# Performance work log

Hardware: AMD Instinct MI355X
Metric: run time of the kernel (lower is better)

## Reference

```python
import jax, jax.numpy as jnp
import numpy as np

# config (mirrors init_kwargs)
R = 1.0           # ball-query radius
K = 32            # ball-query neighbors
SPATIAL_STRIDE = 4
TKS = 3           # temporal kernel size (odd)
TPAD = (1, 1)     # replicate temporal padding
HEADS = 8
DIM_HEAD = 64
DIM = 512
MLP = 2048
DEPTH = 2
LN_EPS = 1e-5


def fps(xyz, m):
    # CUDA-style furthest point sampling, starts at index 0. xyz: [N,3] -> [m] int32
    N = xyz.shape[0]
    def body(carry, _):
        dists, last = carry
        d = jnp.sum((xyz - xyz[last]) ** 2, axis=-1)
        dists = jnp.minimum(dists, d)
        nxt = jnp.argmax(dists).astype(jnp.int32)
        return (dists, nxt), nxt
    init = (jnp.full((N,), 1e10, xyz.dtype), jnp.int32(0))
    _, idxs = jax.lax.scan(body, init, None, length=m - 1)
    return jnp.concatenate([jnp.zeros((1,), jnp.int32), idxs])


def ball_query(neighbor_xyz, anchor_xyz):
    # first K neighbor indices within radius R (pad with first found, 0 if none)
    N = neighbor_xyz.shape[0]
    d2 = jnp.sum((anchor_xyz[:, None, :] - neighbor_xyz[None, :, :]) ** 2, -1)  # [M,N]
    cand = jnp.where(d2 < R * R, jnp.arange(N, dtype=jnp.int32)[None, :], N)
    firstk = jnp.sort(cand, axis=-1)[:, :K]
    first = firstk[:, :1]
    idx = jnp.where(firstk >= N, first, firstk)
    return jnp.where(idx >= N, 0, idx).astype(jnp.int32)


def layer_norm(x, g, b):
    mu = jnp.mean(x, -1, keepdims=True)
    var = jnp.var(x, -1, keepdims=True)
    return (x - mu) * jax.lax.rsqrt(var + LN_EPS) * g + b


def p4dconv(xyzs, Wd):
    # tube embedding: FPS anchors + ball-query grouping + 1x1 conv on (dx,dy,dz,dt)
    B, T, N, _ = xyzs.shape
    pad = jnp.concatenate([xyzs[:, :1]] * TPAD[0] + [xyzs] + [xyzs[:, -1:]] * TPAD[1], axis=1)
    Lp = pad.shape[1]
    m = N // SPATIAL_STRIDE
    half = TKS // 2
    new_xyzs, new_feats = [], []
    for t in range(half, Lp - half, 1):  # temporal_stride = 1
        frame = pad[:, t]                                  # [B,N,3]
        aidx = jax.vmap(lambda x: fps(x, m))(frame)        # [B,m]
        anchor = jax.vmap(lambda f, ix: f[ix])(frame, aidx)  # [B,m,3]
        feats_t = []
        for i in range(t - half, t + half + 1):
            nb = pad[:, i]                                 # [B,N,3]
            idx = jax.vmap(ball_query)(nb, anchor)         # [B,m,K]
            grouped = jax.vmap(lambda n, ix: n[ix])(nb, idx)  # [B,m,K,3]
            disp = grouped - anchor[:, :, None, :]
            tdisp = jnp.full((B, m, K, 1), float(i - t), disp.dtype)
            d4 = jnp.concatenate([disp, tdisp], -1)        # [B,m,K,4]
            f = jnp.einsum('bmkf,cf->bmkc', d4, Wd)        # 1x1 conv, no bias/BN/act
            feats_t.append(jnp.max(f, axis=2))             # spatial max pool
        new_feats.append(jnp.max(jnp.stack(feats_t, 1), axis=1))  # temporal max pool
        new_xyzs.append(anchor)
    return jnp.stack(new_xyzs, 1), jnp.stack(new_feats, 1)  # [B,L,m,3], [B,L,m,C]


def attention(xyzs, feats, Wqkv, Wsp, Wout, bout, g, b):
    B, L, n, C = feats.shape
    M = L * n
    x = layer_norm(feats, g, b)
    qkv = jnp.einsum('blnc,ec->blne', x, Wqkv).reshape(B, M, 3, HEADS, DIM_HEAD)
    q, k, v = [jnp.transpose(qkv[:, :, j], (0, 2, 1, 3)) for j in range(3)]  # [B,h,M,d]
    dots = jnp.einsum('bhid,bhjd->bhij', q, k) * (DIM_HEAD ** -0.5)
    attn = jax.nn.softmax(dots, axis=-1)
    out_v = jnp.einsum('bhij,bhjd->bhid', attn, v)
    xyz_f = xyzs.reshape(B, M, 3)
    delta = xyz_f[:, None, :, :] - xyz_f[:, :, None, :]      # [B,i,j,3] = xyz_j - xyz_i
    wdelta = jnp.einsum('bhij,bijc->bhic', attn, delta)      # attn-weighted displacement
    disp_f = jnp.einsum('bhic,dc->bhid', wdelta, Wsp)        # spatial_op Linear(3->d)
    out = out_v + disp_f
    out = jnp.transpose(out, (0, 2, 1, 3)).reshape(B, M, HEADS * DIM_HEAD)
    out = jax.nn.gelu(out @ Wout.T + bout, approximate=False)
    return out.reshape(B, L, n, C) + feats


def feed_forward(x, g, b, W1, b1, W2, b2):
    h = layer_norm(x, g, b)
    h = jax.nn.gelu(h @ W1.T + b1, approximate=False)
    return h @ W2.T + b2 + x


def setup_inputs() -> dict:
    key = jax.random.key(0)
    ks = jax.random.split(key, 12)
    s = 0.02
    inner = HEADS * DIM_HEAD
    return {
        'xyzs': jax.random.normal(ks[0], (2, 4, 1024, 3), jnp.float32),
        'Wd': jax.random.normal(ks[1], (DIM, 4), jnp.float32) * s,
        'Wqkv': jax.random.normal(ks[2], (DEPTH, 3 * inner, DIM), jnp.float32) * s,
        'Wsp': jax.random.normal(ks[3], (DEPTH, DIM_HEAD, 3), jnp.float32) * s,
        'Wout': jax.random.normal(ks[4], (DEPTH, DIM, inner), jnp.float32) * s,
        'bout': jnp.zeros((DEPTH, DIM), jnp.float32),
        'ln1_g': jnp.ones((DEPTH, DIM), jnp.float32),
        'ln1_b': jnp.zeros((DEPTH, DIM), jnp.float32),
        'Wff1': jax.random.normal(ks[5], (DEPTH, MLP, DIM), jnp.float32) * s,
        'bff1': jnp.zeros((DEPTH, MLP), jnp.float32),
        'Wff2': jax.random.normal(ks[6], (DEPTH, DIM, MLP), jnp.float32) * s,
        'bff2': jnp.zeros((DEPTH, DIM), jnp.float32),
        'ln2_g': jnp.ones((DEPTH, DIM), jnp.float32),
        'ln2_b': jnp.zeros((DEPTH, DIM), jnp.float32),
    }


def reference(xyzs, Wd, Wqkv, Wsp, Wout, bout, ln1_g, ln1_b, Wff1, bff1, Wff2, bff2, ln2_g, ln2_b):
    new_xyzs, feats = p4dconv(xyzs, Wd)   # [B,L,m,3], [B,L,m,DIM]
    feats = jax.nn.relu(feats)            # emb_relu after tube embedding
    for i in range(DEPTH):
        feats = attention(new_xyzs, feats, Wqkv[i], Wsp[i], Wout[i], bout[i], ln1_g[i], ln1_b[i])
        feats = feed_forward(feats, ln2_g[i], ln2_b[i], Wff1[i], bff1[i], Wff2[i], bff2[i])
    return feats
```

## Files before the change

kernel.cpp:

```cpp
#include <hip/hip_runtime.h>
#include <math.h>
#include <stdint.h>


typedef __bf16 bf16_t;
typedef __bf16 bf16x8 __attribute__((ext_vector_type(8)));
typedef __bf16 bf16x4 __attribute__((ext_vector_type(4)));
typedef float f32x4 __attribute__((ext_vector_type(4)));

__device__ __forceinline__ void async16(const bf16_t* g, bf16_t* l) {
  __builtin_amdgcn_global_load_lds(
      (const __attribute__((address_space(1))) void*)g,
      (__attribute__((address_space(3))) void*)l, 16, 0, 0);
}

__device__ __forceinline__ float wave_max_dpp(float v) {
  int a = __float_as_int(v);
  int t;
  t = __builtin_amdgcn_update_dpp(a, a, 0x111, 0xf, 0xf, false);
  a = __float_as_int(fmaxf(__int_as_float(a), __int_as_float(t)));
  t = __builtin_amdgcn_update_dpp(a, a, 0x112, 0xf, 0xf, false);
  a = __float_as_int(fmaxf(__int_as_float(a), __int_as_float(t)));
  t = __builtin_amdgcn_update_dpp(a, a, 0x114, 0xf, 0xf, false);
  a = __float_as_int(fmaxf(__int_as_float(a), __int_as_float(t)));
  t = __builtin_amdgcn_update_dpp(a, a, 0x118, 0xf, 0xf, false);
  a = __float_as_int(fmaxf(__int_as_float(a), __int_as_float(t)));
  t = __builtin_amdgcn_update_dpp(a, a, 0x142, 0xf, 0xf, false);
  a = __float_as_int(fmaxf(__int_as_float(a), __int_as_float(t)));
  t = __builtin_amdgcn_update_dpp(a, a, 0x143, 0xf, 0xf, false);
  a = __float_as_int(fmaxf(__int_as_float(a), __int_as_float(t)));
  return __int_as_float(a);
}

template <int CTRL>
__device__ __forceinline__ unsigned long long dpp_max_u64(unsigned long long kv) {
  uint32_t lo = (uint32_t)kv, hi = (uint32_t)(kv >> 32);
  uint32_t lo2 =
      (uint32_t)__builtin_amdgcn_update_dpp((int)lo, (int)lo, CTRL, 0xf, 0xf, false);
  uint32_t hi2 =
      (uint32_t)__builtin_amdgcn_update_dpp((int)hi, (int)hi, CTRL, 0xf, 0xf, false);
  unsigned long long other = ((unsigned long long)hi2 << 32) | lo2;
  return other > kv ? other : kv;
}

__global__ __launch_bounds__(512) void fps_kernel(const float* __restrict__ xyzs,
                                                  float* __restrict__ anchors) {
  int bid = blockIdx.x;
  int to = bid & 3, b = bid >> 2;
  const float* fr = xyzs + (size_t)(b * 4 + to) * 1024 * 3;
  float* an = anchors + (size_t)(b * 4 + to) * 256 * 3;
  __shared__ __align__(16) float4 sp[1024];
  __shared__ __align__(16) unsigned long long keys[2][8];
  int tid = threadIdx.x;
  int w = tid >> 6, lane = tid & 63;
  float px[2], py[2], pz[2], dist[2];
#pragma unroll
  for (int r = 0; r < 2; ++r) {
    int i = r * 512 + tid;
    float x = fr[i * 3 + 0], y = fr[i * 3 + 1], z = fr[i * 3 + 2];
    px[r] = x; py[r] = y; pz[r] = z; dist[r] = 1e10f;
    sp[i] = make_float4(x, y, z, 0.0f);
  }
  __syncthreads();
  float4 c = sp[0];
  if (tid == 0) { an[0] = c.x; an[1] = c.y; an[2] = c.z; }
  for (int s = 1; s < 256; ++s) {
    int par = s & 1;
#pragma unroll
    for (int r = 0; r < 2; ++r) {
      float dx = px[r] - c.x, dy = py[r] - c.y, dz = pz[r] - c.z;
      float d = fmaf(dx, dx, fmaf(dy, dy, dz * dz));
      dist[r] = fminf(dist[r], d);
    }
    float mloc = fmaxf(dist[0], dist[1]);
    float wmax = wave_max_dpp(mloc);
    float smax = __int_as_float(__builtin_amdgcn_readlane(__float_as_int(wmax), 63));
    unsigned int cidx = 0xFFFFFFFFu;
#pragma unroll
    for (int r = 1; r >= 0; --r) {
      unsigned long long m = __ballot(dist[r] == smax);
      unsigned int tz = (unsigned int)__builtin_ctzll(m | 0x8000000000000000ull);
      unsigned int cand = (unsigned int)(r * 512 + w * 64) + tz;
      cidx = m ? cand : cidx;
    }
    unsigned long long key =
        ((unsigned long long)__float_as_uint(smax) << 32) |
        (unsigned long long)(~cidx);
    if (lane == 0) keys[par][w] = key;
    __syncthreads();
    unsigned long long kv = keys[par][lane & 7];
    kv = dpp_max_u64<0xB1>(kv);
    kv = dpp_max_u64<0x4E>(kv);
    kv = dpp_max_u64<0x124>(kv);
    unsigned int bi = ~(unsigned int)(kv & 0xFFFFFFFFull);
    c = sp[bi];
    if (tid == 0) { an[s * 3 + 0] = c.x; an[s * 3 + 1] = c.y; an[s * 3 + 2] = c.z; }
  }
}

__global__ __launch_bounds__(192) void conv_kernel(
    const float* __restrict__ xyzs, const float* __restrict__ anchors,
    const float* __restrict__ Wd, float* __restrict__ feats) {
  int bid = blockIdx.x;
  int j = bid & 255, to = (bid >> 8) & 3, b = bid >> 10;
  __shared__ float disp[96][4];
  __shared__ int idxbuf[3][32];
  const float* an = anchors + (size_t)((b * 4 + to) * 256 + j) * 3;
  float ax = an[0], ay = an[1], az = an[2];
  int w = threadIdx.x >> 6, lane = threadIdx.x & 63;
  int src = to + w - 1; src = src < 0 ? 0 : (src > 3 ? 3 : src);
  const float* nb = xyzs + (size_t)(b * 4 + src) * 1024 * 3;
  int cnt = 0;
  for (int ch = 0; ch < 16; ++ch) {
    if (cnt >= 32) break;
    int i = ch * 64 + lane;
    float dx = ax - nb[i * 3], dy = ay - nb[i * 3 + 1], dz = az - nb[i * 3 + 2];
    float d2 = dx * dx + dy * dy + dz * dz;
    bool in = d2 < 1.0f;
    unsigned long long mask = __ballot(in);
    if (in) {
      int pos = cnt + (int)__popcll(mask & ((1ull << lane) - 1ull));
      if (pos < 32) idxbuf[w][pos] = i;
    }
    cnt += (int)__popcll(mask);
  }
  if (cnt > 32) cnt = 32;
  if (lane >= cnt && lane < 32) idxbuf[w][lane] = (cnt > 0) ? idxbuf[w][0] : 0;
  if (lane < 32) {
    int ni = idxbuf[w][lane];
    int row = w * 32 + lane;
    disp[row][0] = nb[ni * 3 + 0] - ax;
    disp[row][1] = nb[ni * 3 + 1] - ay;
    disp[row][2] = nb[ni * 3 + 2] - az;
    disp[row][3] = (float)(w - 1);
  }
  __syncthreads();
  float* fout = feats + ((size_t)(b * 1024) + to * 256 + j) * 512;
  for (int c = threadIdx.x; c < 512; c += 192) {
    const float* wr = Wd + c * 4;
    float w0 = wr[0], w1 = wr[1], w2 = wr[2], w3 = wr[3];
    float mx = -1e30f;
#pragma unroll 8
    for (int nn = 0; nn < 96; ++nn) {
      float v = disp[nn][0] * w0 + disp[nn][1] * w1 + disp[nn][2] * w2 + disp[nn][3] * w3;
      mx = fmaxf(mx, v);
    }
    fout[c] = fmaxf(mx, 0.0f);
  }
}

__global__ __launch_bounds__(256) void cvt_all_kernel(
    const float* __restrict__ s0, bf16_t* __restrict__ d0,
    const float* __restrict__ s1, bf16_t* __restrict__ d1,
    const float* __restrict__ s2, bf16_t* __restrict__ d2,
    const float* __restrict__ s3, bf16_t* __restrict__ d3) {
  int idx = blockIdx.x * 256 + threadIdx.x;
  const float* s; bf16_t* d; int off;
  if (idx < 393216) { s = s0; d = d0; off = idx; }
  else if (idx < 524288) { s = s1; d = d1; off = idx - 393216; }
  else if (idx < 1048576) { s = s2; d = d2; off = idx - 524288; }
  else { s = s3; d = d3; off = idx - 1048576; }
  float4 v = ((const float4*)s)[off];
  bf16x4 o = {(bf16_t)v.x, (bf16_t)v.y, (bf16_t)v.z, (bf16_t)v.w};
  ((bf16x4*)d)[off] = o;
}

__global__ __launch_bounds__(256) void ln_kernel(
    const float* __restrict__ x, const float* __restrict__ g,
    const float* __restrict__ bt, bf16_t* __restrict__ y) {
  int row = blockIdx.x;
  int tid = threadIdx.x;
  const float* xr = x + (size_t)row * 512;
  float v0 = xr[tid], v1 = xr[tid + 256];
  float s = v0 + v1;
#pragma unroll
  for (int off = 32; off >= 1; off >>= 1) s += __shfl_xor(s, off, 64);
  __shared__ float red1[4], red2[4];
  int w = tid >> 6, lane = tid & 63;
  if (lane == 0) red1[w] = s;
  __syncthreads();
  float mu = (red1[0] + red1[1] + red1[2] + red1[3]) * (1.0f / 512.0f);
  float d0 = v0 - mu, d1 = v1 - mu;
  float q = d0 * d0 + d1 * d1;
#pragma unroll
  for (int off = 32; off >= 1; off >>= 1) q += __shfl_xor(q, off, 64);
  if (lane == 0) red2[w] = q;
  __syncthreads();
  float var = (red2[0] + red2[1] + red2[2] + red2[3]) * (1.0f / 512.0f);
  float rs = rsqrtf(var + 1e-5f);
  bf16_t* yr = y + (size_t)row * 512;
  yr[tid] = (bf16_t)(d0 * rs * g[tid] + bt[tid]);
  yr[tid + 256] = (bf16_t)(d1 * rs * g[tid + 256] + bt[tid + 256]);
}

template <int BM, int BN, bool GELU, bool BIAS, bool RES, bool OUTBF>
__global__ __launch_bounds__(256) void gemm_bf16(
    const bf16_t* __restrict__ A, const bf16_t* __restrict__ W,
    const float* __restrict__ bias, const float* __restrict__ res,
    void* __restrict__ Cout, int Mn, int Nn, int Kn) {
  constexpr int BK = 32;
  constexpr int WM = BM / 2, WN = BN / 2;
  constexpr int MT = WM / 16, NT = WN / 16;
  constexpr int APW = (BM / 16) / 4;
  constexpr int BPW = (BN / 16) / 4;
  __shared__ __align__(16) bf16_t As[BM * BK];
  __shared__ __align__(16) bf16_t Bs[BN * BK];
  int tid = threadIdx.x;
  int w = tid >> 6, lane = tid & 63;
  int wr = w >> 1, wc = w & 1;
  int m0 = blockIdx.y * BM, n0 = blockIdx.x * BN;
  int lrow = lane >> 2;
  int lk8 = (lane & 3) * 8;
  f32x4 acc[MT][NT] = {};

  const int a_fo = (wr * WM + (lane & 15)) * BK + (lane >> 4) * 8;
  const int b_fo = (wc * WN + (lane & 15)) * BK + (lane >> 4) * 8;

  for (int k0 = 0; k0 < Kn; k0 += BK) {
    __syncthreads();
#pragma unroll
    for (int i = 0; i < APW; ++i) {
      int g = w + i * 4;
      const bf16_t* gp = A + ((size_t)(m0 + g * 16 + lrow) * Kn + k0 + lk8);
      async16(gp, As + g * 16 * BK);
    }
#pragma unroll
    for (int i = 0; i < BPW; ++i) {
      int g = w + i * 4;
      const bf16_t* gp = W + ((size_t)(n0 + g * 16 + lrow) * Kn + k0 + lk8);
      async16(gp, Bs + g * 16 * BK);
    }
    __syncthreads();
    bf16x8 aF[MT], bF[NT];
#pragma unroll
    for (int mt = 0; mt < MT; ++mt)
      aF[mt] = *(const bf16x8*)&As[a_fo + mt * 16 * BK];
#pragma unroll
    for (int nt = 0; nt < NT; ++nt)
      bF[nt] = *(const bf16x8*)&Bs[b_fo + nt * 16 * BK];
#pragma unroll
    for (int mt = 0; mt < MT; ++mt)
#pragma unroll
      for (int nt = 0; nt < NT; ++nt)
        acc[mt][nt] = __builtin_amdgcn_mfma_f32_16x16x32_bf16(
            aF[mt], bF[nt], acc[mt][nt], 0, 0, 0);
  }
  int rbase = (lane >> 4) * 4;
  int col_l = lane & 15;
#pragma unroll
  for (int mt = 0; mt < MT; ++mt) {
#pragma unroll
    for (int reg = 0; reg < 4; ++reg) {
      int r = m0 + wr * WM + mt * 16 + rbase + reg;
      size_t roff = (size_t)r * Nn;
#pragma unroll
      for (int nt = 0; nt < NT; ++nt) {
        int c = n0 + wc * WN + nt * 16 + col_l;
        float v = acc[mt][nt][reg];
        if (BIAS) v += bias[c];
        if (GELU) v = v * 0.5f * (1.0f + erff(v * 0.7071067811865475f));
        if (RES) v += res[roff + c];
        if (OUTBF) ((bf16_t*)Cout)[roff + c] = (bf16_t)v;
        else ((float*)Cout)[roff + c] = v;
      }
    }
  }
}

__global__ __launch_bounds__(256) void attn_kernel(
    const bf16_t* __restrict__ qkv, const float* __restrict__ xyzf,
    const float* __restrict__ Wsp, bf16_t* __restrict__ outp) {
  int bid = blockIdx.x;
  int qt = bid & 15, h = (bid >> 4) & 7, b = bid >> 7;
  int tid = threadIdx.x;
  int w = tid >> 6, lane = tid & 63;
  int l15 = lane & 15, quad = lane >> 4;

  __shared__ __align__(16) bf16_t Kb[64 * 64];
  __shared__ __align__(16) bf16_t Vt[64 * 72];
  __shared__ __align__(16) bf16_t Ps[4][16 * 72];
  __shared__ __align__(16) float4 Xs[64];

  const size_t tokbase = (size_t)b * 1024;
  int qbase = qt * 64 + w * 16;

  bf16x8 aQ[2];
  {
    const bf16_t* qp = qkv + (tokbase + qbase + l15) * 1536 + h * 64 + quad * 8;
    aQ[0] = *(const bf16x8*)(qp);
    aQ[1] = *(const bf16x8*)(qp + 32);
  }

  f32x4 oacc[4] = {};
  float lr[4] = {}, pxr[4] = {}, pyr[4] = {}, pzr[4] = {};

  for (int ch = 0; ch < 16; ++ch) {
    int j0 = ch * 64;
    __syncthreads();
    {
      int r0 = tid >> 3, seg = tid & 7;
      const bf16_t* g0 = qkv + (tokbase + j0 + r0) * 1536 + 512 + h * 64 + seg * 8;
      async16(g0, Kb + tid * 8);
      const bf16_t* g1 = qkv + (tokbase + j0 + 32 + r0) * 1536 + 512 + h * 64 + seg * 8;
      async16(g1, Kb + 2048 + tid * 8);
    }
#pragma unroll
    for (int t = 0; t < 4; ++t) {
      int task = t * 256 + tid;
      int rp = task >> 5, c2 = task & 31;
      const uint32_t* vsrc = (const uint32_t*)(qkv + (tokbase + j0 + 2 * rp) * 1536 +
                                               1024 + h * 64 + 2 * c2);
      uint32_t a = vsrc[0];
      uint32_t bq = vsrc[768];
      uint32_t wlo = (a & 0xffffu) | (bq << 16);
      uint32_t whi = (a >> 16) | (bq & 0xffff0000u);
      uint32_t* vd = (uint32_t*)Vt;
      vd[c2 * 72 + rp] = wlo;
      vd[c2 * 72 + 36 + rp] = whi;
    }
    if (tid < 64) {
      const float* xp = xyzf + (tokbase + j0 + tid) * 3;
      Xs[tid] = make_float4(xp[0], xp[1], xp[2], 0.0f);
    }
    __syncthreads();
    f32x4 sacc[4] = {};
#pragma unroll
    for (int ks = 0; ks < 2; ++ks)
#pragma unroll
      for (int nt = 0; nt < 4; ++nt) {
        bf16x8 bK = *(const bf16x8*)&Kb[(nt * 16 + l15) * 64 + ks * 32 + quad * 8];
        sacc[nt] = __builtin_amdgcn_mfma_f32_16x16x32_bf16(aQ[ks], bK, sacc[nt], 0, 0, 0);
      }
#pragma unroll
    for (int nt = 0; nt < 4; ++nt) {
      float4 xk = Xs[nt * 16 + l15];
#pragma unroll
      for (int reg = 0; reg < 4; ++reg) {
        float p = __expf(sacc[nt][reg] * 0.125f);
        bf16_t pb = (bf16_t)p;
        float pf = (float)pb;
        Ps[w][(quad * 4 + reg) * 72 + nt * 16 + l15] = pb;
        lr[reg] += pf;
        pxr[reg] = fmaf(pf, xk.x, pxr[reg]);
        pyr[reg] = fmaf(pf, xk.y, pyr[reg]);
        pzr[reg] = fmaf(pf, xk.z, pzr[reg]);
      }
    }
    bf16x8 aP[2];
    aP[0] = *(const bf16x8*)&Ps[w][l15 * 72 + quad * 8];
    aP[1] = *(const bf16x8*)&Ps[w][l15 * 72 + 32 + quad * 8];
#pragma unroll
    for (int ks = 0; ks < 2; ++ks)
#pragma unroll
      for (int ct = 0; ct < 4; ++ct) {
        bf16x8 bV = *(const bf16x8*)&Vt[(ct * 16 + l15) * 72 + ks * 32 + quad * 8];
        oacc[ct] = __builtin_amdgcn_mfma_f32_16x16x32_bf16(aP[ks], bV, oacc[ct], 0, 0, 0);
      }
  }
#pragma unroll
  for (int reg = 0; reg < 4; ++reg) {
#pragma unroll
    for (int off = 1; off <= 8; off <<= 1) {
      lr[reg] += __shfl_xor(lr[reg], off, 64);
      pxr[reg] += __shfl_xor(pxr[reg], off, 64);
      pyr[reg] += __shfl_xor(pyr[reg], off, 64);
      pzr[reg] += __shfl_xor(pzr[reg], off, 64);
    }
  }
#pragma unroll
  for (int reg = 0; reg < 4; ++reg) {
    size_t tok = tokbase + qbase + quad * 4 + reg;
    float inv = 1.0f / lr[reg];
    const float* xqp = xyzf + tok * 3;
    float wd0 = pxr[reg] * inv - xqp[0];
    float wd1 = pyr[reg] * inv - xqp[1];
    float wd2 = pzr[reg] * inv - xqp[2];
#pragma unroll
    for (int ct = 0; ct < 4; ++ct) {
      int c = ct * 16 + l15;
      const float* wr = Wsp + c * 3;
      float dv = wd0 * wr[0] + wd1 * wr[1] + wd2 * wr[2];
      outp[tok * 512 + h * 64 + c] = (bf16_t)(oacc[ct][reg] * inv + dv);
    }
  }
}

extern "C" void kernel_launch(void* const* d_in, const int* in_sizes, int n_in,
                              void* d_out, int out_size, void* d_ws, size_t ws_size,
                              hipStream_t stream) {
  const float* xyzs = (const float*)d_in[0];
  const float* Wd   = (const float*)d_in[1];
  const float* Wqkv = (const float*)d_in[2];
  const float* Wsp  = (const float*)d_in[3];
  const float* Wout = (const float*)d_in[4];
  const float* bout = (const float*)d_in[5];
  const float* ln1g = (const float*)d_in[6];
  const float* ln1b = (const float*)d_in[7];
  const float* Wff1 = (const float*)d_in[8];
  const float* bff1 = (const float*)d_in[9];
  const float* Wff2 = (const float*)d_in[10];
  const float* bff2 = (const float*)d_in[11];
  const float* ln2g = (const float*)d_in[12];
  const float* ln2b = (const float*)d_in[13];
  float* out = (float*)d_out;

  float* ws = (float*)d_ws;
  float* anchors = ws;
  float* featsA  = ws + 8192;
  float* featsB  = featsA + 1048576;
  float* big     = featsB + 1048576;
  bf16_t* bigb   = (bf16_t*)big;
  bf16_t* xlnb   = (bf16_t*)(big + 3145728);
  bf16_t* attob  = xlnb + 1048576;
  bf16_t* wq_b   = attob + 1048576;
  bf16_t* wo_b   = wq_b + 1572864;
  bf16_t* w1_b   = wo_b + 524288;
  bf16_t* w2_b   = w1_b + 2097152;

  fps_kernel<<<8, 512, 0, stream>>>(xyzs, anchors);
  cvt_all_kernel<<<6144, 256, 0, stream>>>(Wqkv, wq_b, Wout, wo_b,
                                           Wff1, w1_b, Wff2, w2_b);
  conv_kernel<<<2048, 192, 0, stream>>>(xyzs, anchors, Wd, featsA);

  for (int dep = 0; dep < 2; ++dep) {
    ln_kernel<<<2048, 256, 0, stream>>>(featsA, ln1g + dep * 512, ln1b + dep * 512, xlnb);
    gemm_bf16<128, 128, false, false, false, true><<<dim3(12, 16), 256, 0, stream>>>(
        xlnb, wq_b + (size_t)dep * 786432, nullptr, nullptr, bigb, 2048, 1536, 512);
    attn_kernel<<<256, 256, 0, stream>>>(bigb, anchors, Wsp + dep * 192, attob);
    gemm_bf16<64, 64, true, true, true, false><<<dim3(8, 32), 256, 0, stream>>>(
        attob, wo_b + (size_t)dep * 262144, bout + dep * 512, featsA, featsB,
        2048, 512, 512);
    ln_kernel<<<2048, 256, 0, stream>>>(featsB, ln2g + dep * 512, ln2b + dep * 512, xlnb);
    gemm_bf16<128, 128, true, true, false, true><<<dim3(16, 16), 256, 0, stream>>>(
        xlnb, w1_b + (size_t)dep * 1048576, bff1 + dep * 2048, nullptr, bigb,
        2048, 2048, 512);
    float* dst = (dep == 1) ? out : featsA;
    gemm_bf16<64, 64, false, true, true, false><<<dim3(8, 32), 256, 0, stream>>>(
        bigb, w2_b + (size_t)dep * 1048576, bff2 + dep * 512, featsB, dst,
        2048, 512, 2048);
  }
}
```

Before: 474.0 us.

## Fuse FPS with weight conversion, double-buffer attention, retile GEMMs with BK=64

Merges the weight fp32->bf16 conversion into the FPS launch as extra blocks so the conversion overlaps the serial FPS blocks. FPS now carries candidate coordinates through the DPP tournament instead of reading the winner from a shared-memory point table. The attention kernel double-buffers its K/V/xyz staging so the next chunk loads while the current one is computed. GEMMs use BK=64 with coalesced row-chunk loads and smaller BM tiles to launch more blocks. The cost is more registers and shared memory per block, plus more DPP operations per FPS step.

```diff
diff --git a/kernel.cpp b/kernel.cpp
--- a/kernel.cpp
+++ b/kernel.cpp
@@ -33,42 +33,67 @@
 }
 
 template <int CTRL>
-__device__ __forceinline__ unsigned long long dpp_max_u64(unsigned long long kv) {
+__device__ __forceinline__ void tourney(unsigned long long& kv, float& x,
+                                        float& y, float& z) {
   uint32_t lo = (uint32_t)kv, hi = (uint32_t)(kv >> 32);
   uint32_t lo2 =
       (uint32_t)__builtin_amdgcn_update_dpp((int)lo, (int)lo, CTRL, 0xf, 0xf, false);
   uint32_t hi2 =
       (uint32_t)__builtin_amdgcn_update_dpp((int)hi, (int)hi, CTRL, 0xf, 0xf, false);
+  float x2 = __int_as_float(__builtin_amdgcn_update_dpp(
+      __float_as_int(x), __float_as_int(x), CTRL, 0xf, 0xf, false));
+  float y2 = __int_as_float(__builtin_amdgcn_update_dpp(
+      __float_as_int(y), __float_as_int(y), CTRL, 0xf, 0xf, false));
+  float z2 = __int_as_float(__builtin_amdgcn_update_dpp(
+      __float_as_int(z), __float_as_int(z), CTRL, 0xf, 0xf, false));
   unsigned long long other = ((unsigned long long)hi2 << 32) | lo2;
-  return other > kv ? other : kv;
-}
-
-__global__ __launch_bounds__(512) void fps_kernel(const float* __restrict__ xyzs,
-                                                  float* __restrict__ anchors) {
+  bool take = other > kv;
+  kv = take ? other : kv;
+  x = take ? x2 : x;
+  y = take ? y2 : y;
+  z = take ? z2 : z;
+}
+
+__global__ __launch_bounds__(512) void fps_cvt_kernel(
+    const float* __restrict__ xyzs, float* __restrict__ anchors,
+    const float* __restrict__ s0, bf16_t* __restrict__ d0,
+    const float* __restrict__ s1, bf16_t* __restrict__ d1,
+    const float* __restrict__ s2, bf16_t* __restrict__ d2,
+    const float* __restrict__ s3, bf16_t* __restrict__ d3) {
   int bid = blockIdx.x;
+  int tid = threadIdx.x;
+  if (bid >= 8) {
+    int idx = (bid - 8) * 512 + tid;
+    const float* s; bf16_t* d; int off;
+    if (idx < 393216) { s = s0; d = d0; off = idx; }
+    else if (idx < 524288) { s = s1; d = d1; off = idx - 393216; }
+    else if (idx < 1048576) { s = s2; d = d2; off = idx - 524288; }
+    else { s = s3; d = d3; off = idx - 1048576; }
+    float4 v = ((const float4*)s)[off];
+    bf16x4 o = {(bf16_t)v.x, (bf16_t)v.y, (bf16_t)v.z, (bf16_t)v.w};
+    ((bf16x4*)d)[off] = o;
+    return;
+  }
   int to = bid & 3, b = bid >> 2;
   const float* fr = xyzs + (size_t)(b * 4 + to) * 1024 * 3;
   float* an = anchors + (size_t)(b * 4 + to) * 256 * 3;
-  __shared__ __align__(16) float4 sp[1024];
+  __shared__ __align__(16) float4 cand[2][8];
   __shared__ __align__(16) unsigned long long keys[2][8];
-  int tid = threadIdx.x;
   int w = tid >> 6, lane = tid & 63;
   float px[2], py[2], pz[2], dist[2];
 #pragma unroll
   for (int r = 0; r < 2; ++r) {
     int i = r * 512 + tid;
-    float x = fr[i * 3 + 0], y = fr[i * 3 + 1], z = fr[i * 3 + 2];
-    px[r] = x; py[r] = y; pz[r] = z; dist[r] = 1e10f;
-    sp[i] = make_float4(x, y, z, 0.0f);
-  }
-  __syncthreads();
-  float4 c = sp[0];
-  if (tid == 0) { an[0] = c.x; an[1] = c.y; an[2] = c.z; }
+    px[r] = fr[i * 3 + 0]; py[r] = fr[i * 3 + 1]; pz[r] = fr[i * 3 + 2];
+    dist[r] = 1e10f;
+  }
+  float cx = fr[0], cy = fr[1], cz = fr[2];
+  if (tid == 0) { an[0] = cx; an[1] = cy; an[2] = cz; }
   for (int s = 1; s < 256; ++s) {
     int par = s & 1;
 #pragma unroll
     for (int r = 0; r < 2; ++r) {
-      float dx = px[r] - c.x, dy = py[r] - c.y, dz = pz[r] - c.z;
+      float dx = px[r] - cx, dy = py[r] - cy, dz = pz[r] - cz;
       float d = fmaf(dx, dx, fmaf(dy, dy, dz * dz));
       dist[r] = fminf(dist[r], d);
     }
@@ -80,21 +105,27 @@
     for (int r = 1; r >= 0; --r) {
       unsigned long long m = __ballot(dist[r] == smax);
       unsigned int tz = (unsigned int)__builtin_ctzll(m | 0x8000000000000000ull);
-      unsigned int cand = (unsigned int)(r * 512 + w * 64) + tz;
-      cidx = m ? cand : cidx;
+      unsigned int candi = (unsigned int)(r * 512 + w * 64) + tz;
+      cidx = m ? candi : cidx;
     }
     unsigned long long key =
         ((unsigned long long)__float_as_uint(smax) << 32) |
         (unsigned long long)(~cidx);
+    int wl = (int)(cidx & 63u), rsel = (int)(cidx >> 9);
+    if (lane == wl) {
+      cand[par][w] = make_float4(rsel ? px[1] : px[0], rsel ? py[1] : py[0],
+                                 rsel ? pz[1] : pz[0], 0.0f);
+    }
     if (lane == 0) keys[par][w] = key;
     __syncthreads();
     unsigned long long kv = keys[par][lane & 7];
-    kv = dpp_max_u64<0xB1>(kv);
-    kv = dpp_max_u64<0x4E>(kv);
-    kv = dpp_max_u64<0x124>(kv);
-    unsigned int bi = ~(unsigned int)(kv & 0xFFFFFFFFull);
-    c = sp[bi];
-    if (tid == 0) { an[s * 3 + 0] = c.x; an[s * 3 + 1] = c.y; an[s * 3 + 2] = c.z; }
+    float4 cd = cand[par][lane & 7];
+    float tx = cd.x, ty = cd.y, tz2 = cd.z;
+    tourney<0xB1>(kv, tx, ty, tz2);
+    tourney<0x4E>(kv, tx, ty, tz2);
+    tourney<0x124>(kv, tx, ty, tz2);
+    cx = tx; cy = ty; cz = tz2;
+    if (tid == 0) { an[s * 3 + 0] = cx; an[s * 3 + 1] = cy; an[s * 3 + 2] = cz; }
   }
 }
 
@@ -149,22 +180,6 @@
   }
 }
 
-__global__ __launch_bounds__(256) void cvt_all_kernel(
-    const float* __restrict__ s0, bf16_t* __restrict__ d0,
-    const float* __restrict__ s1, bf16_t* __restrict__ d1,
-    const float* __restrict__ s2, bf16_t* __restrict__ d2,
-    const float* __restrict__ s3, bf16_t* __restrict__ d3) {
-  int idx = blockIdx.x * 256 + threadIdx.x;
-  const float* s; bf16_t* d; int off;
-  if (idx < 393216) { s = s0; d = d0; off = idx; }
-  else if (idx < 524288) { s = s1; d = d1; off = idx - 393216; }
-  else if (idx < 1048576) { s = s2; d = d2; off = idx - 524288; }
-  else { s = s3; d = d3; off = idx - 1048576; }
-  float4 v = ((const float4*)s)[off];
-  bf16x4 o = {(bf16_t)v.x, (bf16_t)v.y, (bf16_t)v.z, (bf16_t)v.w};
-  ((bf16x4*)d)[off] = o;
-}
-
 __global__ __launch_bounds__(256) void ln_kernel(
     const float* __restrict__ x, const float* __restrict__ g,
     const float* __restrict__ bt, bf16_t* __restrict__ y) {
@@ -198,55 +213,56 @@
     const bf16_t* __restrict__ A, const bf16_t* __restrict__ W,
     const float* __restrict__ bias, const float* __restrict__ res,
     void* __restrict__ Cout, int Mn, int Nn, int Kn) {
-  constexpr int BK = 32;
+  constexpr int BK = 64;
   constexpr int WM = BM / 2, WN = BN / 2;
   constexpr int MT = WM / 16, NT = WN / 16;
-  constexpr int APW = (BM / 16) / 4;
-  constexpr int BPW = (BN / 16) / 4;
+  constexpr int AIT = (BM * BK / 8) / 256;
+  constexpr int BIT = (BN * BK / 8) / 256;
   __shared__ __align__(16) bf16_t As[BM * BK];
   __shared__ __align__(16) bf16_t Bs[BN * BK];
   int tid = threadIdx.x;
   int w = tid >> 6, lane = tid & 63;
   int wr = w >> 1, wc = w & 1;
   int m0 = blockIdx.y * BM, n0 = blockIdx.x * BN;
-  int lrow = lane >> 2;
-  int lk8 = (lane & 3) * 8;
+  int l15 = lane & 15, quad = lane >> 4;
   f32x4 acc[MT][NT] = {};
 
-  const int a_fo = (wr * WM + (lane & 15)) * BK + (lane >> 4) * 8;
-  const int b_fo = (wc * WN + (lane & 15)) * BK + (lane >> 4) * 8;
+  const int a_fo = (wr * WM + l15) * BK + quad * 8;
+  const int b_fo = (wc * WN + l15) * BK + quad * 8;
 
   for (int k0 = 0; k0 < Kn; k0 += BK) {
     __syncthreads();
 #pragma unroll
-    for (int i = 0; i < APW; ++i) {
-      int g = w + i * 4;
-      const bf16_t* gp = A + ((size_t)(m0 + g * 16 + lrow) * Kn + k0 + lk8);
-      async16(gp, As + g * 16 * BK);
-    }
-#pragma unroll
-    for (int i = 0; i < BPW; ++i) {
-      int g = w + i * 4;
-      const bf16_t* gp = W + ((size_t)(n0 + g * 16 + lrow) * Kn + k0 + lk8);
-      async16(gp, Bs + g * 16 * BK);
+    for (int i = 0; i < AIT; ++i) {
+      int chunk = i * 256 + tid;
+      int row = chunk >> 3, c8 = chunk & 7;
+      async16(A + ((size_t)(m0 + row) * Kn + k0 + c8 * 8), As + chunk * 8);
+    }
+#pragma unroll
+    for (int i = 0; i < BIT; ++i) {
+      int chunk = i * 256 + tid;
+      int row = chunk >> 3, c8 = chunk & 7;
+      async16(W + ((size_t)(n0 + row) * Kn + k0 + c8 * 8), Bs + chunk * 8);
     }
     __syncthreads();
-    bf16x8 aF[MT], bF[NT];
-#pragma unroll
-    for (int mt = 0; mt < MT; ++mt)
-      aF[mt] = *(const bf16x8*)&As[a_fo + mt * 16 * BK];
-#pragma unroll
-    for (int nt = 0; nt < NT; ++nt)
-      bF[nt] = *(const bf16x8*)&Bs[b_fo + nt * 16 * BK];
-#pragma unroll
-    for (int mt = 0; mt < MT; ++mt)
+#pragma unroll
+    for (int ks = 0; ks < 2; ++ks) {
+      bf16x8 aF[MT], bF[NT];
+#pragma unroll
+      for (int mt = 0; mt < MT; ++mt)
+        aF[mt] = *(const bf16x8*)&As[a_fo + mt * 16 * BK + ks * 32];
 #pragma unroll
       for (int nt = 0; nt < NT; ++nt)
-        acc[mt][nt] = __builtin_amdgcn_mfma_f32_16x16x32_bf16(
-            aF[mt], bF[nt], acc[mt][nt], 0, 0, 0);
-  }
-  int rbase = (lane >> 4) * 4;
-  int col_l = lane & 15;
+        bF[nt] = *(const bf16x8*)&Bs[b_fo + nt * 16 * BK + ks * 32];
+#pragma unroll
+      for (int mt = 0; mt < MT; ++mt)
+#pragma unroll
+        for (int nt = 0; nt < NT; ++nt)
+          acc[mt][nt] = __builtin_amdgcn_mfma_f32_16x16x32_bf16(
+              aF[mt], bF[nt], acc[mt][nt], 0, 0, 0);
+    }
+  }
+  int rbase = quad * 4;
 #pragma unroll
   for (int mt = 0; mt < MT; ++mt) {
 #pragma unroll
@@ -255,7 +271,7 @@
       size_t roff = (size_t)r * Nn;
 #pragma unroll
       for (int nt = 0; nt < NT; ++nt) {
-        int c = n0 + wc * WN + nt * 16 + col_l;
+        int c = n0 + wc * WN + nt * 16 + l15;
         float v = acc[mt][nt][reg];
         if (BIAS) v += bias[c];
         if (GELU) v = v * 0.5f * (1.0f + erff(v * 0.7071067811865475f));
@@ -276,10 +292,10 @@
   int w = tid >> 6, lane = tid & 63;
   int l15 = lane & 15, quad = lane >> 4;
 
-  __shared__ __align__(16) bf16_t Kb[64 * 64];
-  __shared__ __align__(16) bf16_t Vt[64 * 72];
+  __shared__ __align__(16) bf16_t Kb[2][64 * 64];
+  __shared__ __align__(16) bf16_t Vt[2][64 * 72];
   __shared__ __align__(16) bf16_t Ps[4][16 * 72];
-  __shared__ __align__(16) float4 Xs[64];
+  __shared__ __align__(16) float4 Xs[2][64];
 
   const size_t tokbase = (size_t)b * 1024;
   int qbase = qt * 64 + w * 16;
@@ -294,16 +310,13 @@
   f32x4 oacc[4] = {};
   float lr[4] = {}, pxr[4] = {}, pyr[4] = {}, pzr[4] = {};
 
-  for (int ch = 0; ch < 16; ++ch) {
+  auto stage = [&](int ch, int buf) {
     int j0 = ch * 64;
-    __syncthreads();
-    {
-      int r0 = tid >> 3, seg = tid & 7;
-      const bf16_t* g0 = qkv + (tokbase + j0 + r0) * 1536 + 512 + h * 64 + seg * 8;
-      async16(g0, Kb + tid * 8);
-      const bf16_t* g1 = qkv + (tokbase + j0 + 32 + r0) * 1536 + 512 + h * 64 + seg * 8;
-      async16(g1, Kb + 2048 + tid * 8);
-    }
+    int r0 = tid >> 3, seg = tid & 7;
+    const bf16_t* g0 = qkv + (tokbase + j0 + r0) * 1536 + 512 + h * 64 + seg * 8;
+    async16(g0, Kb[buf] + tid * 8);
+    const bf16_t* g1 = qkv + (tokbase + j0 + 32 + r0) * 1536 + 512 + h * 64 + seg * 8;
+    async16(g1, Kb[buf] + 2048 + tid * 8);
 #pragma unroll
     for (int t = 0; t < 4; ++t) {
       int task = t * 256 + tid;
@@ -314,26 +327,32 @@
       uint32_t bq = vsrc[768];
       uint32_t wlo = (a & 0xffffu) | (bq << 16);
       uint32_t whi = (a >> 16) | (bq & 0xffff0000u);
-      uint32_t* vd = (uint32_t*)Vt;
+      uint32_t* vd = (uint32_t*)Vt[buf];
       vd[c2 * 72 + rp] = wlo;
       vd[c2 * 72 + 36 + rp] = whi;
     }
     if (tid < 64) {
       const float* xp = xyzf + (tokbase + j0 + tid) * 3;
-      Xs[tid] = make_float4(xp[0], xp[1], xp[2], 0.0f);
-    }
+      Xs[buf][tid] = make_float4(xp[0], xp[1], xp[2], 0.0f);
+    }
+  };
+
+  stage(0, 0);
+  for (int ch = 0; ch < 16; ++ch) {
+    int cur = ch & 1;
     __syncthreads();
+    if (ch + 1 < 16) stage(ch + 1, cur ^ 1);
     f32x4 sacc[4] = {};
 #pragma unroll
     for (int ks = 0; ks < 2; ++ks)
 #pragma unroll
       for (int nt = 0; nt < 4; ++nt) {
-        bf16x8 bK = *(const bf16x8*)&Kb[(nt * 16 + l15) * 64 + ks * 32 + quad * 8];
+        bf16x8 bK = *(const bf16x8*)&Kb[cur][(nt * 16 + l15) * 64 + ks * 32 + quad * 8];
         sacc[nt] = __builtin_amdgcn_mfma_f32_16x16x32_bf16(aQ[ks], bK, sacc[nt], 0, 0, 0);
       }
 #pragma unroll
     for (int nt = 0; nt < 4; ++nt) {
-      float4 xk = Xs[nt * 16 + l15];
+      float4 xk = Xs[cur][nt * 16 + l15];
 #pragma unroll
       for (int reg = 0; reg < 4; ++reg) {
         float p = __expf(sacc[nt][reg] * 0.125f);
@@ -353,7 +372,7 @@
     for (int ks = 0; ks < 2; ++ks)
 #pragma unroll
       for (int ct = 0; ct < 4; ++ct) {
-        bf16x8 bV = *(const bf16x8*)&Vt[(ct * 16 + l15) * 72 + ks * 32 + quad * 8];
+        bf16x8 bV = *(const bf16x8*)&Vt[cur][(ct * 16 + l15) * 72 + ks * 32 + quad * 8];
         oacc[ct] = __builtin_amdgcn_mfma_f32_16x16x32_bf16(aP[ks], bV, oacc[ct], 0, 0, 0);
       }
   }
@@ -417,25 +436,24 @@
   bf16_t* w1_b   = wo_b + 524288;
   bf16_t* w2_b   = w1_b + 2097152;
 
-  fps_kernel<<<8, 512, 0, stream>>>(xyzs, anchors);
-  cvt_all_kernel<<<6144, 256, 0, stream>>>(Wqkv, wq_b, Wout, wo_b,
+  fps_cvt_kernel<<<3080, 512, 0, stream>>>(xyzs, anchors, Wqkv, wq_b, Wout, wo_b,
                                            Wff1, w1_b, Wff2, w2_b);
   conv_kernel<<<2048, 192, 0, stream>>>(xyzs, anchors, Wd, featsA);
 
   for (int dep = 0; dep < 2; ++dep) {
     ln_kernel<<<2048, 256, 0, stream>>>(featsA, ln1g + dep * 512, ln1b + dep * 512, xlnb);
-    gemm_bf16<128, 128, false, false, false, true><<<dim3(12, 16), 256, 0, stream>>>(
+    gemm_bf16<64, 128, false, false, false, true><<<dim3(12, 32), 256, 0, stream>>>(
         xlnb, wq_b + (size_t)dep * 786432, nullptr, nullptr, bigb, 2048, 1536, 512);
     attn_kernel<<<256, 256, 0, stream>>>(bigb, anchors, Wsp + dep * 192, attob);
-    gemm_bf16<64, 64, true, true, true, false><<<dim3(8, 32), 256, 0, stream>>>(
+    gemm_bf16<32, 64, true, true, true, false><<<dim3(8, 64), 256, 0, stream>>>(
         attob, wo_b + (size_t)dep * 262144, bout + dep * 512, featsA, featsB,
         2048, 512, 512);
     ln_kernel<<<2048, 256, 0, stream>>>(featsB, ln2g + dep * 512, ln2b + dep * 512, xlnb);
-    gemm_bf16<128, 128, true, true, false, true><<<dim3(16, 16), 256, 0, stream>>>(
+    gemm_bf16<64, 128, true, true, false, true><<<dim3(16, 32), 256, 0, stream>>>(
         xlnb, w1_b + (size_t)dep * 1048576, bff1 + dep * 2048, nullptr, bigb,
         2048, 2048, 512);
     float* dst = (dep == 1) ? out : featsA;
-    gemm_bf16<64, 64, false, true, true, false><<<dim3(8, 32), 256, 0, stream>>>(
+    gemm_bf16<32, 64, false, true, true, false><<<dim3(8, 64), 256, 0, stream>>>(
         bigb, w2_b + (size_t)dep * 1048576, bff2 + dep * 512, featsB, dst,
         2048, 512, 2048);
   }
```

Result: no change. 466.5 us (-1.6%).
